# Kernel tuning notes

Hardware: AMD Instinct MI355X
Metric: run time of the kernel (lower is better)

## Reference

```python
import jax, jax.numpy as jnp
import numpy as np

B, L, C = 2, 2048, 1024
H = 16
HD = C // H  # head_features = 64


def setup_inputs() -> dict:
    key = jax.random.key(0)
    k1, k2, k3, k4, k5, k6 = jax.random.split(key, 6)
    input_x = jax.random.normal(k1, (B, L, C), dtype=jnp.float32)
    x_mask = jax.random.randint(k2, (B, 1, 1, L), 0, 2, dtype=jnp.int32)
    s = 1.0 / np.sqrt(C)
    W_qkv = jax.random.normal(k3, (C, 3 * C), dtype=jnp.float32) * s
    b_qkv = jax.random.normal(k4, (3 * C,), dtype=jnp.float32) * 0.01
    W_proj = jax.random.normal(k5, (C, C), dtype=jnp.float32) * s
    b_proj = jax.random.normal(k6, (C,), dtype=jnp.float32) * 0.01
    return {"input_x": input_x, "x_mask": x_mask, "W_qkv": W_qkv,
            "b_qkv": b_qkv, "W_proj": W_proj, "b_proj": b_proj}


def reference(input_x, x_mask, W_qkv, b_qkv, W_proj, b_proj):
    # qkv projection: [B,L,3C] -> [3,B,H,L,HD]
    qkv = input_x @ W_qkv + b_qkv
    qkv = qkv.reshape(B, L, 3, H, HD).transpose(2, 0, 3, 1, 4)
    q, k, v = qkv[0], qkv[1], qkv[2]
    q = q * (HD ** -0.5)  # first scale (module applies it to q)
    scores = jnp.einsum('bhld,bhmd->bhlm', q, k)  # [B,H,L,L]
    scores = jnp.where(x_mask == 1, jnp.float32(-1e10), scores)
    scores = scores / jnp.sqrt(jnp.float32(HD))  # module's second scale (faithful quirk)
    probs = jax.nn.softmax(scores, axis=-1)
    out = jnp.einsum('bhlm,bhmd->bhld', probs, v)  # [B,H,L,HD]
    out = out.transpose(0, 2, 1, 3).reshape(B, L, C)
    return out @ W_proj + b_proj
```

## Files before the change

kernel.cpp:

```cpp
#include <hip/hip_runtime.h>
#include <stdint.h>

typedef __attribute__((ext_vector_type(8))) short short8;
typedef __attribute__((ext_vector_type(4))) short short4v;
typedef __attribute__((ext_vector_type(4))) float floatx4;
typedef __attribute__((ext_vector_type(16))) float floatx16;

#define B_ 2
#define L_ 2048
#define C_ 1024
#define H_ 16
#define HD_ 64

#define QSCALE (0.015625f * 1.44269504088896f)
#define MASKVAL (-1.8033688e9f)

__device__ __forceinline__ unsigned short f2bf(float f) {
  union { float f; uint32_t u; } v; v.f = f;
  uint32_t r = 0x7FFFu + ((v.u >> 16) & 1u);
  return (unsigned short)((v.u + r) >> 16);
}

__device__ __forceinline__ uint32_t cvtpk(float lo, float hi) {
  uint32_t r;
  asm("v_cvt_pk_bf16_f32 %0, %1, %2" : "=v"(r) : "v"(lo), "v"(hi));
  return r;
}

__device__ __forceinline__ void pl32swap(uint32_t& a, uint32_t& b) {
  asm volatile("v_permlane32_swap_b32 %0, %1" : "+v"(a), "+v"(b));
}

__device__ __forceinline__ void async16(const void* g, void* l) {
  __builtin_amdgcn_global_load_lds(
      (const __attribute__((address_space(1))) void*)g,
      (__attribute__((address_space(3))) void*)l, 16, 0, 0);
}

__global__ __launch_bounds__(256) void cast_bf16_k(const float* __restrict__ in,
                                                   unsigned short* __restrict__ out, int n) {
  int i = (blockIdx.x * 256 + threadIdx.x) * 8;
  if (i >= n) return;
  floatx4 a = *(const floatx4*)(in + i);
  floatx4 b = *(const floatx4*)(in + i + 4);
  short8 o;
  o[0] = (short)f2bf(a[0]); o[1] = (short)f2bf(a[1]);
  o[2] = (short)f2bf(a[2]); o[3] = (short)f2bf(a[3]);
  o[4] = (short)f2bf(b[0]); o[5] = (short)f2bf(b[1]);
  o[6] = (short)f2bf(b[2]); o[7] = (short)f2bf(b[3]);
  *(short8*)(out + i) = o;
}

__global__ __launch_bounds__(256) void transpose_cast_k(const float* __restrict__ in,
                                                        unsigned short* __restrict__ out,
                                                        int R, int Cc) {
  __shared__ float tile[32][33];
  int tx = threadIdx.x, ty = threadIdx.y;
  int c0 = blockIdx.x * 32, r0 = blockIdx.y * 32;
#pragma unroll
  for (int i = 0; i < 4; i++)
    tile[ty + i * 8][tx] = in[(r0 + ty + i * 8) * Cc + c0 + tx];
  __syncthreads();
#pragma unroll
  for (int i = 0; i < 4; i++)
    out[(c0 + ty + i * 8) * R + r0 + tx] = f2bf(tile[tx][ty + i * 8]);
}

__global__ __launch_bounds__(256) void maskpre_k(const int* __restrict__ mask,
                                                 float* __restrict__ maskfg) {
  int i = blockIdx.x * 256 + threadIdx.x;
  if (i < B_ * L_) maskfg[i] = (mask[i] == 1) ? MASKVAL : 0.f;
}

template <int EPI>
__global__ __launch_bounds__(256) void gemm128(const unsigned short* __restrict__ A,
                                               const unsigned short* __restrict__ BT, int K,
                                               const float* __restrict__ bias,
                                               unsigned short* __restrict__ outQ,
                                               unsigned short* __restrict__ outK,
                                               unsigned short* __restrict__ outVT,
                                               float* __restrict__ outF) {
  __shared__ __attribute__((aligned(16))) unsigned short Asmem[128 * 32];
  __shared__ __attribute__((aligned(16))) unsigned short Bsmem[128 * 32];
  const int t = threadIdx.x;
  const int wave = t >> 6, lane = t & 63;
  const int wr = wave >> 1, wc = wave & 1;
  const int row0 = blockIdx.y * 128;
  const int col0 = blockIdx.x * 128;
  floatx4 acc[4][4] = {};

  for (int k0 = 0; k0 < K; k0 += 32) {
    __syncthreads();
#pragma unroll
    for (int i = 0; i < 2; i++) {
      int idx = i * 256 + t;
      async16(A + (size_t)(row0 + (idx >> 2)) * K + k0 + (idx & 3) * 8, Asmem + idx * 8);
      async16(BT + (size_t)(col0 + (idx >> 2)) * K + k0 + (idx & 3) * 8, Bsmem + idx * 8);
    }
    __syncthreads();
    short8 af[4], bfr[4];
#pragma unroll
    for (int m = 0; m < 4; m++)
      af[m] = *(const short8*)(Asmem + (wr * 64 + m * 16 + (lane & 15)) * 32 + (lane >> 4) * 8);
#pragma unroll
    for (int n = 0; n < 4; n++)
      bfr[n] = *(const short8*)(Bsmem + (wc * 64 + n * 16 + (lane & 15)) * 32 + (lane >> 4) * 8);
#pragma unroll
    for (int m = 0; m < 4; m++)
#pragma unroll
      for (int n = 0; n < 4; n++)
        acc[m][n] = __builtin_amdgcn_mfma_f32_16x16x32_bf16(af[m], bfr[n], acc[m][n], 0, 0, 0);
  }

#pragma unroll
  for (int m = 0; m < 4; m++)
#pragma unroll
    for (int n = 0; n < 4; n++)
#pragma unroll
      for (int j = 0; j < 4; j++) {
        int r = row0 + wr * 64 + m * 16 + (lane >> 4) * 4 + j;
        int c = col0 + wc * 64 + n * 16 + (lane & 15);
        float v = acc[m][n][j] + bias[c];
        if (EPI == 1) {
          int b = r >> 11, l = r & 2047;
          int which = c >> 10, rem = c & 1023;
          int h = rem >> 6, d = rem & 63;
          size_t base = (size_t)(b * H_ + h) * L_ * HD_;
          if (which == 0)
            outQ[base + (size_t)l * HD_ + d] = f2bf(v * QSCALE);
          else if (which == 1)
            outK[base + ((l >> 5) * 8 + (d >> 4) * 2 + ((d >> 3) & 1)) * 256 +
                 (l & 31) * 8 + (d & 7)] = f2bf(v);
          else
            outVT[base + ((((l >> 7) * 2 + (d >> 5)) * 8 + ((l >> 4) & 7)) * 2 +
                          ((l >> 3) & 1)) * 256 + (d & 31) * 8 + (l & 7)] = f2bf(v);
        } else {
          outF[(size_t)r * C_ + c] = v;
        }
      }
}

__global__ __launch_bounds__(256) void attn_k(const unsigned short* __restrict__ Q,
                                              const unsigned short* __restrict__ Kf,
                                              const unsigned short* __restrict__ VTf,
                                              const float* __restrict__ maskfg,
                                              unsigned short* __restrict__ attn_out) {
  __shared__ __attribute__((aligned(16))) unsigned short Ks[128 * 64];
  __shared__ __attribute__((aligned(16))) unsigned short VTs[64 * 128];
  __shared__ __attribute__((aligned(16))) float maskL[L_];

  const int t = threadIdx.x, wave = t >> 6, lane = t & 63;
  const int h = lane >> 5, c32 = lane & 31;
  const int bh = blockIdx.x & 31;
  const int qt = blockIdx.x >> 5;
  const int b = bh >> 4, hh = bh & 15;
  const unsigned short* Qp = Q + (size_t)bh * L_ * HD_;
  const unsigned short* Kp = Kf + (size_t)bh * L_ * HD_;
  const unsigned short* VTp = VTf + (size_t)bh * L_ * HD_;
  const int qrow = qt * 128 + wave * 32 + c32;

  short8 qf[4];
#pragma unroll
  for (int ks = 0; ks < 4; ks++)
    qf[ks] = *(const short8*)(Qp + (size_t)qrow * HD_ + ks * 16 + h * 8);

#pragma unroll
  for (int i = 0; i < 2; i++) {
    int idx = i * 256 + t;
    async16(maskfg + b * L_ + idx * 4, maskL + idx * 4);
  }

  floatx16 o[2] = {};
  float lrun = 0.f;

  for (int kv = 0; kv < 16; kv++) {
    __syncthreads();
#pragma unroll
    for (int i = 0; i < 4; i++) {
      int idx = i * 256 + t;
      async16(Kp + (size_t)kv * 8192 + idx * 8, Ks + idx * 8);
    }
#pragma unroll
    for (int i = 0; i < 4; i++) {
      int idx = i * 256 + t;
      async16(VTp + (size_t)kv * 8192 + idx * 8, VTs + idx * 8);
    }
    __syncthreads();

    floatx16 s[4];
#pragma unroll
    for (int kg = 0; kg < 4; kg++) {
#pragma unroll
      for (int rr = 0; rr < 4; rr++) {
        floatx4 mk = *(const floatx4*)(maskL + kv * 128 + kg * 32 + rr * 8 + h * 4);
#pragma unroll
        for (int jj = 0; jj < 4; jj++) s[kg][rr * 4 + jj] = mk[jj];
      }
#pragma unroll
      for (int ks = 0; ks < 4; ks++) {
        const short8 kfr = *(const short8*)(Ks + ((kg * 4 + ks) * 2 + h) * 256 + c32 * 8);
        s[kg] = __builtin_amdgcn_mfma_f32_32x32x16_bf16(kfr, qf[ks], s[kg], 0, 0, 0);
      }
    }

    float rs = 0.f;
#pragma unroll
    for (int kg = 0; kg < 4; kg++)
#pragma unroll
      for (int e = 0; e < 16; e++) {
        float p = __builtin_amdgcn_exp2f(s[kg][e]);
        s[kg][e] = p;
        rs += p;
      }
    rs += __shfl_xor(rs, 32);
    lrun += rs;

#pragma unroll
    for (int kg = 0; kg < 4; kg++) {
      uint32_t pk[8];
#pragma unroll
      for (int e = 0; e < 8; e++) pk[e] = cvtpk(s[kg][2 * e], s[kg][2 * e + 1]);
#pragma unroll
      for (int ts = 0; ts < 2; ts++) {
        uint32_t x0 = pk[4 * ts + 0], x1 = pk[4 * ts + 1];
        uint32_t y0 = pk[4 * ts + 2], y1 = pk[4 * ts + 3];
        pl32swap(x0, y0);
        pl32swap(x1, y1);
        union { uint32_t u[4]; short8 v; } pf;
        pf.u[0] = x0; pf.u[1] = x1; pf.u[2] = y0; pf.u[3] = y1;
        const int kt = kg * 2 + ts;
#pragma unroll
        for (int dg = 0; dg < 2; dg++) {
          const short8 vfr = *(const short8*)(VTs + ((dg * 8 + kt) * 2 + h) * 256 + c32 * 8);
          o[dg] = __builtin_amdgcn_mfma_f32_32x32x16_bf16(vfr, pf.v, o[dg], 0, 0, 0);
        }
      }
    }
  }

  const float inv = 1.f / lrun;
#pragma unroll
  for (int dg = 0; dg < 2; dg++)
#pragma unroll
    for (int rr = 0; rr < 4; rr++) {
      short4v ov;
#pragma unroll
      for (int jj = 0; jj < 4; jj++) ov[jj] = (short)f2bf(o[dg][rr * 4 + jj] * inv);
      int d0 = dg * 32 + rr * 8 + h * 4;
      *(short4v*)(attn_out + ((size_t)b * L_ + qrow) * C_ + hh * HD_ + d0) = ov;
    }
}

extern "C" void kernel_launch(void* const* d_in, const int* in_sizes, int n_in,
                              void* d_out, int out_size, void* d_ws, size_t ws_size,
                              hipStream_t stream) {
  const float* x = (const float*)d_in[0];
  const int* mask = (const int*)d_in[1];
  const float* Wqkv = (const float*)d_in[2];
  const float* bqkv = (const float*)d_in[3];
  const float* Wproj = (const float*)d_in[4];
  const float* bproj = (const float*)d_in[5];
  float* out = (float*)d_out;
  char* ws = (char*)d_ws;

  unsigned short* Xb = (unsigned short*)(ws);
  unsigned short* WqkvT = (unsigned short*)(ws + (8u << 20));
  unsigned short* WprojT = (unsigned short*)(ws + (14u << 20));
  unsigned short* Qb = (unsigned short*)(ws + (16u << 20));
  unsigned short* Kb = (unsigned short*)(ws + (24u << 20));
  unsigned short* VTb = (unsigned short*)(ws + (32u << 20));
  unsigned short* AOb = Xb;
  float* maskfg = (float*)(ws + (8u << 20));

  cast_bf16_k<<<(B_ * L_ * C_) / 8 / 256, 256, 0, stream>>>(x, Xb, B_ * L_ * C_);
  dim3 tb(32, 8);
  transpose_cast_k<<<dim3(3 * C_ / 32, C_ / 32), tb, 0, stream>>>(Wqkv, WqkvT, C_, 3 * C_);
  transpose_cast_k<<<dim3(C_ / 32, C_ / 32), tb, 0, stream>>>(Wproj, WprojT, C_, C_);

  gemm128<1><<<dim3(3 * C_ / 128, B_ * L_ / 128), 256, 0, stream>>>(
      Xb, WqkvT, C_, bqkv, Qb, Kb, VTb, nullptr);

  maskpre_k<<<(B_ * L_) / 256, 256, 0, stream>>>(mask, maskfg);

  attn_k<<<B_ * H_ * (L_ / 128), 256, 0, stream>>>(Qb, Kb, VTb, maskfg, AOb);

  gemm128<2><<<dim3(C_ / 128, B_ * L_ / 128), 256, 0, stream>>>(
      AOb, WprojT, C_, bproj, nullptr, nullptr, nullptr, out);
}
```

Measured before the change: 129.0 us.

## Double-buffer GEMM LDS tiles, remap blocks across XCDs, vectorize QKV epilogue stores

The GEMM kernel now uses two LDS buffers so the async global-to-LDS loads for the next K slice are issued while MFMAs run on the current one, with a single barrier per iteration. Blocks are launched on a 1D grid and remapped so consecutive tiles land on the same XCD, which should improve L2 reuse. The epilogue hoists index math out of the inner loop, uses the hardware bf16 convert, and writes V^T as a packed 4-element store. The cost is double the LDS per block and an extra 1D-to-2D index computation.

Result: faster. 121.4 us (-5.9%).

```diff
diff --git a/kernel.cpp b/kernel.cpp
--- a/kernel.cpp
+++ b/kernel.cpp
@@ -25,6 +25,10 @@
   uint32_t r;
   asm("v_cvt_pk_bf16_f32 %0, %1, %2" : "=v"(r) : "v"(lo), "v"(hi));
   return r;
+}
+
+__device__ __forceinline__ unsigned short f2bf_hw(float f) {
+  return (unsigned short)cvtpk(f, f);
 }
 
 __device__ __forceinline__ void pl32swap(uint32_t& a, uint32_t& b) {
@@ -75,69 +79,96 @@
 template <int EPI>
 __global__ __launch_bounds__(256) void gemm128(const unsigned short* __restrict__ A,
                                                const unsigned short* __restrict__ BT, int K,
+                                               int nbx,
                                                const float* __restrict__ bias,
                                                unsigned short* __restrict__ outQ,
                                                unsigned short* __restrict__ outK,
                                                unsigned short* __restrict__ outVT,
                                                float* __restrict__ outF) {
-  __shared__ __attribute__((aligned(16))) unsigned short Asmem[128 * 32];
-  __shared__ __attribute__((aligned(16))) unsigned short Bsmem[128 * 32];
+  __shared__ __attribute__((aligned(16))) unsigned short Asmem[2][128 * 32];
+  __shared__ __attribute__((aligned(16))) unsigned short Bsmem[2][128 * 32];
   const int t = threadIdx.x;
   const int wave = t >> 6, lane = t & 63;
   const int wr = wave >> 1, wc = wave & 1;
-  const int row0 = blockIdx.y * 128;
-  const int col0 = blockIdx.x * 128;
+  const int nwg = gridDim.x;
+  const int id = (blockIdx.x & 7) * (nwg >> 3) + (blockIdx.x >> 3);
+  const int bx = id % nbx, by = id / nbx;
+  const int row0 = by * 128, col0 = bx * 128;
+
+  const int arow = row0 + (t >> 2), brow = col0 + (t >> 2);
+  const int koff = (t & 3) * 8;
+
+#define STAGE(buf, k0)                                                               \
+  {                                                                                  \
+    async16(A + (size_t)arow * K + (k0) + koff, &Asmem[buf][t * 8]);                 \
+    async16(A + (size_t)(arow + 64) * K + (k0) + koff, &Asmem[buf][(256 + t) * 8]);  \
+    async16(BT + (size_t)brow * K + (k0) + koff, &Bsmem[buf][t * 8]);                \
+    async16(BT + (size_t)(brow + 64) * K + (k0) + koff, &Bsmem[buf][(256 + t) * 8]); \
+  }
+
   floatx4 acc[4][4] = {};
-
+  STAGE(0, 0);
+  __syncthreads();
+  int cur = 0;
   for (int k0 = 0; k0 < K; k0 += 32) {
-    __syncthreads();
-#pragma unroll
-    for (int i = 0; i < 2; i++) {
-      int idx = i * 256 + t;
-      async16(A + (size_t)(row0 + (idx >> 2)) * K + k0 + (idx & 3) * 8, Asmem + idx * 8);
-      async16(BT + (size_t)(col0 + (idx >> 2)) * K + k0 + (idx & 3) * 8, Bsmem + idx * 8);
-    }
-    __syncthreads();
+    if (k0 + 32 < K) STAGE(cur ^ 1, k0 + 32);
     short8 af[4], bfr[4];
 #pragma unroll
     for (int m = 0; m < 4; m++)
-      af[m] = *(const short8*)(Asmem + (wr * 64 + m * 16 + (lane & 15)) * 32 + (lane >> 4) * 8);
+      af[m] = *(const short8*)(&Asmem[cur][(wr * 64 + m * 16 + (lane & 15)) * 32 +
+                                           (lane >> 4) * 8]);
 #pragma unroll
     for (int n = 0; n < 4; n++)
-      bfr[n] = *(const short8*)(Bsmem + (wc * 64 + n * 16 + (lane & 15)) * 32 + (lane >> 4) * 8);
+      bfr[n] = *(const short8*)(&Bsmem[cur][(wc * 64 + n * 16 + (lane & 15)) * 32 +
+                                            (lane >> 4) * 8]);
 #pragma unroll
     for (int m = 0; m < 4; m++)
 #pragma unroll
       for (int n = 0; n < 4; n++)
         acc[m][n] = __builtin_amdgcn_mfma_f32_16x16x32_bf16(af[m], bfr[n], acc[m][n], 0, 0, 0);
+    __syncthreads();
+    cur ^= 1;
   }
+#undef STAGE
 
 #pragma unroll
   for (int m = 0; m < 4; m++)
 #pragma unroll
-    for (int n = 0; n < 4; n++)
-#pragma unroll
-      for (int j = 0; j < 4; j++) {
-        int r = row0 + wr * 64 + m * 16 + (lane >> 4) * 4 + j;
-        int c = col0 + wc * 64 + n * 16 + (lane & 15);
-        float v = acc[m][n][j] + bias[c];
-        if (EPI == 1) {
-          int b = r >> 11, l = r & 2047;
-          int which = c >> 10, rem = c & 1023;
-          int h = rem >> 6, d = rem & 63;
-          size_t base = (size_t)(b * H_ + h) * L_ * HD_;
-          if (which == 0)
-            outQ[base + (size_t)l * HD_ + d] = f2bf(v * QSCALE);
-          else if (which == 1)
-            outK[base + ((l >> 5) * 8 + (d >> 4) * 2 + ((d >> 3) & 1)) * 256 +
-                 (l & 31) * 8 + (d & 7)] = f2bf(v);
-          else
-            outVT[base + ((((l >> 7) * 2 + (d >> 5)) * 8 + ((l >> 4) & 7)) * 2 +
-                          ((l >> 3) & 1)) * 256 + (d & 31) * 8 + (l & 7)] = f2bf(v);
+    for (int n = 0; n < 4; n++) {
+      const int r0e = row0 + wr * 64 + m * 16 + (lane >> 4) * 4;
+      const int cc = col0 + wc * 64 + n * 16 + (lane & 15);
+      const float bv = bias[cc];
+      if (EPI == 2) {
+#pragma unroll
+        for (int j = 0; j < 4; j++)
+          outF[(size_t)(r0e + j) * C_ + cc] = acc[m][n][j] + bv;
+      } else {
+        const int which = col0 >> 10;
+        const int rem = cc & 1023, h = rem >> 6, d = rem & 63;
+        const int bb = r0e >> 11, l0 = r0e & 2047;
+        const size_t base = (size_t)(bb * H_ + h) * (L_ * HD_);
+        if (which == 0) {
+#pragma unroll
+          for (int j = 0; j < 4; j++)
+            outQ[base + (size_t)(l0 + j) * HD_ + d] = f2bf_hw((acc[m][n][j] + bv) * QSCALE);
+        } else if (which == 1) {
+          const size_t kbase =
+              base + ((l0 >> 5) * 8 + (d >> 4) * 2 + ((d >> 3) & 1)) * 256 + (d & 7);
+#pragma unroll
+          for (int j = 0; j < 4; j++)
+            outK[kbase + ((l0 & 31) + j) * 8] = f2bf_hw(acc[m][n][j] + bv);
         } else {
-          outF[(size_t)r * C_ + c] = v;
+          const size_t vbase = base +
+                               ((((l0 >> 7) * 2 + (d >> 5)) * 8 + ((l0 >> 4) & 7)) * 2 +
+                                ((l0 >> 3) & 1)) * 256 +
+                               (d & 31) * 8 + (l0 & 7);
+          union { unsigned short s[4]; short4v v; } ov;
+#pragma unroll
+          for (int j = 0; j < 4; j++) ov.s[j] = f2bf_hw(acc[m][n][j] + bv);
+          *(short4v*)(outVT + vbase) = ov.v;
         }
       }
+    }
 }
 
 __global__ __launch_bounds__(256) void attn_k(const unsigned short* __restrict__ Q,
@@ -277,13 +308,11 @@
   transpose_cast_k<<<dim3(3 * C_ / 32, C_ / 32), tb, 0, stream>>>(Wqkv, WqkvT, C_, 3 * C_);
   transpose_cast_k<<<dim3(C_ / 32, C_ / 32), tb, 0, stream>>>(Wproj, WprojT, C_, C_);
 
-  gemm128<1><<<dim3(3 * C_ / 128, B_ * L_ / 128), 256, 0, stream>>>(
-      Xb, WqkvT, C_, bqkv, Qb, Kb, VTb, nullptr);
+  gemm128<1><<<768, 256, 0, stream>>>(Xb, WqkvT, C_, 24, bqkv, Qb, Kb, VTb, nullptr);
 
   maskpre_k<<<(B_ * L_) / 256, 256, 0, stream>>>(mask, maskfg);
 
   attn_k<<<B_ * H_ * (L_ / 128), 256, 0, stream>>>(Qb, Kb, VTb, maskfg, AOb);
 
-  gemm128<2><<<dim3(C_ / 128, B_ * L_ / 128), 256, 0, stream>>>(
-      AOb, WprojT, C_, bproj, nullptr, nullptr, nullptr, out);
-}
+  gemm128<2><<<256, 256, 0, stream>>>(AOb, WprojT, C_, 8, bproj, nullptr, nullptr, nullptr, out);
+}
```
